# Kernel optimization log

Hardware: AMD Instinct MI355X
Metric: run time of the kernel (lower is better)

## Reference

```python
import jax, jax.numpy as jnp
import numpy as np

VALUE_DIM = 512
VALUE_SIZE = 262144
NUM_LABELS = 64
C = 256
B, T = 4, 1024


def setup_inputs() -> dict:
    key = jax.random.key(0)
    k1, k2, k3, k4, k5 = jax.random.split(key, 5)
    indices = jax.random.randint(k1, (B, T), 0, VALUE_SIZE, dtype=jnp.int64 if jax.config.jax_enable_x64 else jnp.int32)
    scores = jax.random.normal(k2, (B, T), dtype=jnp.float32)
    W = jax.random.normal(k3, (NUM_LABELS, VALUE_DIM, C), dtype=jnp.float32)
    label = jax.random.randint(k4, (B, T), 0, NUM_LABELS, dtype=jnp.int32)
    weight = jax.random.normal(k5, (VALUE_SIZE, VALUE_DIM), dtype=jnp.float32)
    return {"indices": indices, "scores": scores, "W": W, "label": label, "index": 1, "weight": weight}


def reference(indices, scores, W, label, index, weight):
    half = VALUE_DIM // 2
    if index == 1:
        weight_h = weight[:, half:]          # (V, half)
        W_h = W[:, half:, :]                 # (L, half, C)
    else:
        weight_h = weight[:, :half]
        W_h = W[:, :half, :]
    # gather embeddings: (b, t, half)
    selected_values = weight_h[indices]
    # label-indexed matrix gather: (b, t, half, C)
    expanded_params = W_h[label]
    # fused batched matvec + score weighting + sum over t -> (b, C)
    out = jnp.einsum('btd,btdc,bt->bc', selected_values, expanded_params, scores)
    return out
```

## Files before the change

kernel.cpp:

```cpp
#include <hip/hip_runtime.h>

#define Bdim   4
#define Tdim   1024
#define NLAB   64
#define Cdim   256
#define Ddim   512
#define HALF   256
#define BT     (Bdim*Tdim)
#define NBLK   256

template <bool USE_WS>
__global__ __launch_bounds__(512) void vb_kernel(
    const int*   __restrict__ indices,
    const float* __restrict__ scores,
    const float* __restrict__ W,
    const int*   __restrict__ label,
    const int*   __restrict__ index_p,
    const float* __restrict__ weight,
    float*       __restrict__ dst)
{
    const int l     = blockIdx.x & 63;
    const int chunk = blockIdx.x >> 6;
    const int tid   = threadIdx.x;
    const int lane  = tid & 63;
    const int wave  = tid >> 6;
    const int half  = (index_p[0] == 1) ? HALF : 0;
    const int dglob = half + chunk * 64;

    __shared__ int   s_list[BT];
    __shared__ int   s_count;
    __shared__ float A_red[Bdim][64];
    __shared__ float pool[8192];
    float (*A_part)[Bdim][64]  = (float (*)[Bdim][64])pool;
    float (*P)[Bdim][Cdim]     = (float (*)[Bdim][Cdim])pool;

    if (tid == 0) s_count = 0;
    __syncthreads();

    const int c4 = lane * 4;
    float4 w_pre[8];
    #pragma unroll
    for (int dd = 0; dd < 8; ++dd) {
        int dloc = dd * 8 + wave;
        w_pre[dd] = *(const float4*)(
            W + ((size_t)(l * Ddim + dglob + dloc) * Cdim + c4));
    }

    #pragma unroll
    for (int i = 0; i < 2; ++i) {
        int4 lv = ((const int4*)label)[i * 512 + tid];
        int bt0 = (i * 512 + tid) * 4;
        int lv_arr[4] = {lv.x, lv.y, lv.z, lv.w};
        #pragma unroll
        for (int j = 0; j < 4; ++j) {
            bool m = (lv_arr[j] == l);
            unsigned long long mask = __ballot(m);
            int base_s = 0;
            if (lane == 0 && mask)
                base_s = atomicAdd(&s_count, __popcll(mask));
            base_s = __shfl(base_s, 0, 64);
            if (m) {
                int pre = __popcll(mask & ((1ull << lane) - 1ull));
                s_list[base_s + pre] = bt0 + j;
            }
        }
    }
    __syncthreads();
    const int count = s_count;

    const int q    = lane >> 4;
    const int cl   = lane & 15;
    const int slot = wave * 4 + q;

    float4 acc0 = {0,0,0,0}, acc1 = {0,0,0,0}, acc2 = {0,0,0,0}, acc3 = {0,0,0,0};
    for (int m = slot; m < count; m += 32) {
        int   bt  = s_list[m];
        int   b   = bt >> 10;
        float s   = scores[bt];
        int   idx = indices[bt];
        const float4 w = *(const float4*)(weight + (size_t)idx * Ddim + dglob + cl * 4);
        float s0 = (b == 0) ? s : 0.0f;
        float s1 = (b == 1) ? s : 0.0f;
        float s2 = (b == 2) ? s : 0.0f;
        float s3 = (b == 3) ? s : 0.0f;
        acc0.x += s0 * w.x; acc0.y += s0 * w.y; acc0.z += s0 * w.z; acc0.w += s0 * w.w;
        acc1.x += s1 * w.x; acc1.y += s1 * w.y; acc1.z += s1 * w.z; acc1.w += s1 * w.w;
        acc2.x += s2 * w.x; acc2.y += s2 * w.y; acc2.z += s2 * w.z; acc2.w += s2 * w.w;
        acc3.x += s3 * w.x; acc3.y += s3 * w.y; acc3.z += s3 * w.z; acc3.w += s3 * w.w;
    }
    *(float4*)&A_part[slot][0][cl * 4] = acc0;
    *(float4*)&A_part[slot][1][cl * 4] = acc1;
    *(float4*)&A_part[slot][2][cl * 4] = acc2;
    *(float4*)&A_part[slot][3][cl * 4] = acc3;
    __syncthreads();

    if (tid < 256) {
        int b = tid >> 6, d = tid & 63;
        float s = 0.0f;
        #pragma unroll
        for (int k = 0; k < 32; ++k) s += A_part[k][b][d];
        A_red[b][d] = s;
    }
    __syncthreads();

    float4 acc[Bdim];
    #pragma unroll
    for (int b = 0; b < Bdim; ++b) acc[b] = make_float4(0.f, 0.f, 0.f, 0.f);

    #pragma unroll
    for (int dd = 0; dd < 8; ++dd) {
        int dloc = dd * 8 + wave;
        const float4 wv = w_pre[dd];
        #pragma unroll
        for (int b = 0; b < Bdim; ++b) {
            float a = A_red[b][dloc];
            acc[b].x += a * wv.x;
            acc[b].y += a * wv.y;
            acc[b].z += a * wv.z;
            acc[b].w += a * wv.w;
        }
    }

    #pragma unroll
    for (int b = 0; b < Bdim; ++b)
        *(float4*)&P[wave][b][c4] = acc[b];
    __syncthreads();

    {
        int c  = tid & 255;
        int bh = tid >> 8;
        #pragma unroll
        for (int bb = 0; bb < 2; ++bb) {
            int b = bh * 2 + bb;
            float s = 0.0f;
            #pragma unroll
            for (int w2 = 0; w2 < 8; ++w2) s += P[w2][b][c];
            if (USE_WS) {
                dst[(size_t)blockIdx.x * (Bdim * Cdim) + b * Cdim + c] = s;
            } else {
                atomicAdd(&dst[b * Cdim + c], s);
            }
        }
    }
}

__global__ __launch_bounds__(256) void vb_reduce(
    const float* __restrict__ part,
    float*       __restrict__ out)
{
    const int o = blockIdx.x * 256 + threadIdx.x;
    float s = 0.0f;
    #pragma unroll 8
    for (int k = 0; k < NBLK; ++k)
        s += part[(size_t)k * (Bdim * Cdim) + o];
    out[o] = s;
}

extern "C" void kernel_launch(void* const* d_in, const int* in_sizes, int n_in,
                              void* d_out, int out_size, void* d_ws, size_t ws_size,
                              hipStream_t stream) {
    const int*   indices = (const int*)  d_in[0];
    const float* scores  = (const float*)d_in[1];
    const float* W       = (const float*)d_in[2];
    const int*   label   = (const int*)  d_in[3];
    const int*   index_p = (const int*)  d_in[4];
    const float* weight  = (const float*)d_in[5];
    float*       out     = (float*)d_out;

    const size_t need = (size_t)NBLK * Bdim * Cdim * sizeof(float);
    if (d_ws != nullptr && ws_size >= need) {
        float* part = (float*)d_ws;
        vb_kernel<true><<<dim3(NBLK), dim3(512), 0, stream>>>(
            indices, scores, W, label, index_p, weight, part);
        vb_reduce<<<dim3(4), dim3(256), 0, stream>>>(part, out);
    } else {
        hipMemsetAsync(out, 0, (size_t)out_size * sizeof(float), stream);
        vb_kernel<false><<<dim3(NBLK), dim3(512), 0, stream>>>(
            indices, scores, W, label, index_p, weight, out);
    }
}
```

Baseline: 609.3 us.

## Repartition work per batch and output column slice with shared-memory atomic accumulation

Blocks are now assigned per (batch, 16-column output slice) rather than per (label, 64-dim chunk). Each block scatter-accumulates score-weighted embedding rows into a swizzled per-label shared-memory table using LDS atomics, then contracts that table against its W column slice. This drops the workspace partial buffer and the second reduction kernel. In exchange, every block recomputes the full per-batch gather (16x redundant weight reads across column slices), relies on heavy LDS atomic contention, and reads W with narrow 16-float strided accesses.

```diff
diff --git a/kernel.cpp b/kernel.cpp
--- a/kernel.cpp
+++ b/kernel.cpp
@@ -5,11 +5,12 @@
 #define NLAB   64
 #define Cdim   256
 #define Ddim   512
-#define HALF   256
-#define BT     (Bdim*Tdim)
-#define NBLK   256
+#define HALFD  256
+#define APAD   260
+#define WC     16
+#define NCS    (Cdim/WC)
+#define NBLK   (Bdim*NCS)
 
-template <bool USE_WS>
 __global__ __launch_bounds__(512) void vb_kernel(
     const int*   __restrict__ indices,
     const float* __restrict__ scores,
@@ -17,143 +18,89 @@
     const int*   __restrict__ label,
     const int*   __restrict__ index_p,
     const float* __restrict__ weight,
-    float*       __restrict__ dst)
+    float*       __restrict__ out)
 {
-    const int l     = blockIdx.x & 63;
-    const int chunk = blockIdx.x >> 6;
-    const int tid   = threadIdx.x;
-    const int lane  = tid & 63;
-    const int wave  = tid >> 6;
-    const int half  = (index_p[0] == 1) ? HALF : 0;
-    const int dglob = half + chunk * 64;
+    const int b    = blockIdx.x >> 4;
+    const int cs   = blockIdx.x & 15;
+    const int tid  = threadIdx.x;
+    const int half = (index_p[0] == 1) ? HALFD : 0;
+    const int c0   = cs * WC;
 
-    __shared__ int   s_list[BT];
-    __shared__ int   s_count;
-    __shared__ float A_red[Bdim][64];
-    __shared__ float pool[8192];
-    float (*A_part)[Bdim][64]  = (float (*)[Bdim][64])pool;
-    float (*P)[Bdim][Cdim]     = (float (*)[Bdim][Cdim])pool;
+    __shared__ float A[NLAB][APAD];
+    __shared__ int   s_idx[Tdim];
+    __shared__ float s_sc [Tdim];
+    __shared__ int   s_lb [Tdim];
+    __shared__ float P2[32][WC + 1];
 
-    if (tid == 0) s_count = 0;
-    __syncthreads();
-
-    const int c4 = lane * 4;
-    float4 w_pre[8];
-    #pragma unroll
-    for (int dd = 0; dd < 8; ++dd) {
-        int dloc = dd * 8 + wave;
-        w_pre[dd] = *(const float4*)(
-            W + ((size_t)(l * Ddim + dglob + dloc) * Cdim + c4));
-    }
-
-    #pragma unroll
-    for (int i = 0; i < 2; ++i) {
-        int4 lv = ((const int4*)label)[i * 512 + tid];
-        int bt0 = (i * 512 + tid) * 4;
-        int lv_arr[4] = {lv.x, lv.y, lv.z, lv.w};
-        #pragma unroll
-        for (int j = 0; j < 4; ++j) {
-            bool m = (lv_arr[j] == l);
-            unsigned long long mask = __ballot(m);
-            int base_s = 0;
-            if (lane == 0 && mask)
-                base_s = atomicAdd(&s_count, __popcll(mask));
-            base_s = __shfl(base_s, 0, 64);
-            if (m) {
-                int pre = __popcll(mask & ((1ull << lane) - 1ull));
-                s_list[base_s + pre] = bt0 + j;
-            }
-        }
-    }
-    __syncthreads();
-    const int count = s_count;
-
-    const int q    = lane >> 4;
-    const int cl   = lane & 15;
-    const int slot = wave * 4 + q;
-
-    float4 acc0 = {0,0,0,0}, acc1 = {0,0,0,0}, acc2 = {0,0,0,0}, acc3 = {0,0,0,0};
-    for (int m = slot; m < count; m += 32) {
-        int   bt  = s_list[m];
-        int   b   = bt >> 10;
-        float s   = scores[bt];
-        int   idx = indices[bt];
-        const float4 w = *(const float4*)(weight + (size_t)idx * Ddim + dglob + cl * 4);
-        float s0 = (b == 0) ? s : 0.0f;
-        float s1 = (b == 1) ? s : 0.0f;
-        float s2 = (b == 2) ? s : 0.0f;
-        float s3 = (b == 3) ? s : 0.0f;
-        acc0.x += s0 * w.x; acc0.y += s0 * w.y; acc0.z += s0 * w.z; acc0.w += s0 * w.w;
-        acc1.x += s1 * w.x; acc1.y += s1 * w.y; acc1.z += s1 * w.z; acc1.w += s1 * w.w;
-        acc2.x += s2 * w.x; acc2.y += s2 * w.y; acc2.z += s2 * w.z; acc2.w += s2 * w.w;
-        acc3.x += s3 * w.x; acc3.y += s3 * w.y; acc3.z += s3 * w.z; acc3.w += s3 * w.w;
-    }
-    *(float4*)&A_part[slot][0][cl * 4] = acc0;
-    *(float4*)&A_part[slot][1][cl * 4] = acc1;
-    *(float4*)&A_part[slot][2][cl * 4] = acc2;
-    *(float4*)&A_part[slot][3][cl * 4] = acc3;
-    __syncthreads();
-
-    if (tid < 256) {
-        int b = tid >> 6, d = tid & 63;
-        float s = 0.0f;
-        #pragma unroll
-        for (int k = 0; k < 32; ++k) s += A_part[k][b][d];
-        A_red[b][d] = s;
+    for (int i = tid; i < NLAB * APAD; i += 512) (&A[0][0])[i] = 0.0f;
+    for (int t = tid; t < Tdim; t += 512) {
+        s_idx[t] = indices[b * Tdim + t];
+        s_sc [t] = scores [b * Tdim + t];
+        s_lb [t] = label  [b * Tdim + t];
     }
     __syncthreads();
 
-    float4 acc[Bdim];
+    const int slot = tid >> 4;
+    const int cl   = tid & 15;
+
+    int colo[16];
     #pragma unroll
-    for (int b = 0; b < Bdim; ++b) acc[b] = make_float4(0.f, 0.f, 0.f, 0.f);
-
-    #pragma unroll
-    for (int dd = 0; dd < 8; ++dd) {
-        int dloc = dd * 8 + wave;
-        const float4 wv = w_pre[dd];
+    for (int k = 0; k < 4; ++k) {
         #pragma unroll
-        for (int b = 0; b < Bdim; ++b) {
-            float a = A_red[b][dloc];
-            acc[b].x += a * wv.x;
-            acc[b].y += a * wv.y;
-            acc[b].z += a * wv.z;
-            acc[b].w += a * wv.w;
+        for (int j = 0; j < 4; ++j) {
+            int dj  = cl * 4 + j;
+            int m   = (dj >> 4) + 4 * k;
+            int col = (m << 4) | (((dj & 15) + m) & 15);
+            colo[k * 4 + j] = col;
         }
     }
 
-    #pragma unroll
-    for (int b = 0; b < Bdim; ++b)
-        *(float4*)&P[wave][b][c4] = acc[b];
+    #pragma unroll 2
+    for (int it = 0; it < Tdim / 32; ++it) {
+        int   t   = it * 32 + slot;
+        int   idx = s_idx[t];
+        float s   = s_sc [t];
+        int   l   = s_lb [t];
+        const float* wrow = weight + (size_t)idx * Ddim + half + cl * 4;
+        float4 w0 = *(const float4*)(wrow);
+        float4 w1 = *(const float4*)(wrow + 64);
+        float4 w2 = *(const float4*)(wrow + 128);
+        float4 w3 = *(const float4*)(wrow + 192);
+        float* Arow = &A[l][0];
+        atomicAdd(Arow + colo[ 0], s * w0.x); atomicAdd(Arow + colo[ 1], s * w0.y);
+        atomicAdd(Arow + colo[ 2], s * w0.z); atomicAdd(Arow + colo[ 3], s * w0.w);
+        atomicAdd(Arow + colo[ 4], s * w1.x); atomicAdd(Arow + colo[ 5], s * w1.y);
+        atomicAdd(Arow + colo[ 6], s * w1.z); atomicAdd(Arow + colo[ 7], s * w1.w);
+        atomicAdd(Arow + colo[ 8], s * w2.x); atomicAdd(Arow + colo[ 9], s * w2.y);
+        atomicAdd(Arow + colo[10], s * w2.z); atomicAdd(Arow + colo[11], s * w2.w);
+        atomicAdd(Arow + colo[12], s * w3.x); atomicAdd(Arow + colo[13], s * w3.y);
+        atomicAdd(Arow + colo[14], s * w3.z); atomicAdd(Arow + colo[15], s * w3.w);
+    }
     __syncthreads();
 
-    {
-        int c  = tid & 255;
-        int bh = tid >> 8;
+    const int c_loc = tid & 15;
+    const int dq    = tid >> 4;
+    float acc = 0.0f;
+    #pragma unroll 2
+    for (int l = 0; l < NLAB; ++l) {
+        const float* Wl = W + (((size_t)l * Ddim + half + dq) * Cdim) + c0 + c_loc;
         #pragma unroll
-        for (int bb = 0; bb < 2; ++bb) {
-            int b = bh * 2 + bb;
-            float s = 0.0f;
-            #pragma unroll
-            for (int w2 = 0; w2 < 8; ++w2) s += P[w2][b][c];
-            if (USE_WS) {
-                dst[(size_t)blockIdx.x * (Bdim * Cdim) + b * Cdim + c] = s;
-            } else {
-                atomicAdd(&dst[b * Cdim + c], s);
-            }
+        for (int k = 0; k < 8; ++k) {
+            int d   = dq + 32 * k;
+            int m   = d >> 4;
+            int col = (m << 4) | (((d & 15) + m) & 15);
+            acc += A[l][col] * Wl[(size_t)(32 * k) * Cdim];
         }
     }
-}
+    P2[dq][c_loc] = acc;
+    __syncthreads();
 
-__global__ __launch_bounds__(256) void vb_reduce(
-    const float* __restrict__ part,
-    float*       __restrict__ out)
-{
-    const int o = blockIdx.x * 256 + threadIdx.x;
-    float s = 0.0f;
-    #pragma unroll 8
-    for (int k = 0; k < NBLK; ++k)
-        s += part[(size_t)k * (Bdim * Cdim) + o];
-    out[o] = s;
+    if (tid < WC) {
+        float ssum = 0.0f;
+        #pragma unroll
+        for (int q = 0; q < 32; ++q) ssum += P2[q][tid];
+        out[b * Cdim + c0 + tid] = ssum;
+    }
 }
 
 extern "C" void kernel_launch(void* const* d_in, const int* in_sizes, int n_in,
@@ -167,15 +114,6 @@
     const float* weight  = (const float*)d_in[5];
     float*       out     = (float*)d_out;
 
-    const size_t need = (size_t)NBLK * Bdim * Cdim * sizeof(float);
-    if (d_ws != nullptr && ws_size >= need) {
-        float* part = (float*)d_ws;
-        vb_kernel<true><<<dim3(NBLK), dim3(512), 0, stream>>>(
-            indices, scores, W, label, index_p, weight, part);
-        vb_reduce<<<dim3(4), dim3(256), 0, stream>>>(part, out);
-    } else {
-        hipMemsetAsync(out, 0, (size_t)out_size * sizeof(float), stream);
-        vb_kernel<false><<<dim3(NBLK), dim3(512), 0, stream>>>(
-            indices, scores, W, label, index_p, weight, out);
-    }
+    vb_kernel<<<dim3(NBLK), dim3(512), 0, stream>>>(
+        indices, scores, W, label, index_p, weight, out);
 }
```

Measured after the change: 953.8 us. 1.57x slower.
